# Kernel optimization log

Measured on AMD Instinct MI355X. Metric: run time of the kernel, lower is better.

The kernel has to match this reference:

```python
import jax, jax.numpy as jnp
import numpy as np

# ---- static config (mirrors DRR.__init__ kwargs) ----
NX = NY = NZ = 192            # volume dims
H = W = 192                   # detector height/width
SDR = 300.0                   # source-to-rotation-center distance
DELX = DELY = 2.0             # detector pixel pitch (mm)
X0 = Y0 = 0.0                 # detector offsets
SPACING = (1.0, 1.0, 1.0)     # voxel spacing (mm)
BAM = 1.0                     # bone_attenuation_multiplier
B = 2                         # batch (poses)
N_SUB = H * W // 2            # p_subsample = 0.5


def setup_inputs() -> dict:
    key = jax.random.key(0)
    k1, k2, k3, k4 = jax.random.split(key, 4)
    # CT volume in Hounsfield units, spanning air (-1000) to bone (~2000)
    volume = jax.random.uniform(k1, (NX, NY, NZ), jnp.float32, -1000.0, 2000.0)
    rotations = jax.random.normal(k2, (B, 3), jnp.float32)          # Euler ZYX (rad)
    translations = jax.random.normal(k3, (B, 3), jnp.float32) * 10.0  # mm, near isocenter
    # unique subsampled detector pixel indices (Detector.subsamples[-1])
    subsample_idx = jax.random.permutation(k4, H * W)[:N_SUB].astype(jnp.int32)
    return {"volume": volume, "rotations": rotations,
            "translations": translations, "subsample_idx": subsample_idx}


def _rz(t):
    c, s = jnp.cos(t), jnp.sin(t); z = jnp.zeros_like(t); o = jnp.ones_like(t)
    return jnp.stack([jnp.stack([c, -s, z], -1),
                      jnp.stack([s, c, z], -1),
                      jnp.stack([z, z, o], -1)], -2)


def _ry(t):
    c, s = jnp.cos(t), jnp.sin(t); z = jnp.zeros_like(t); o = jnp.ones_like(t)
    return jnp.stack([jnp.stack([c, z, s], -1),
                      jnp.stack([z, o, z], -1),
                      jnp.stack([-s, z, c], -1)], -2)


def _rx(t):
    c, s = jnp.cos(t), jnp.sin(t); z = jnp.zeros_like(t); o = jnp.ones_like(t)
    return jnp.stack([jnp.stack([o, z, z], -1),
                      jnp.stack([z, c, -s], -1),
                      jnp.stack([z, s, c], -1)], -2)


def _density(volume):
    # DRR.__init__: volume.flip([0]); air/soft/bone HU segmentation + normalization
    vol = jnp.flip(volume, 0)
    soft = (vol > -800.0) & (vol <= 350.0)
    soft_min = jnp.min(jnp.where(soft, vol, jnp.inf))
    d = jnp.where(vol <= -800.0, soft_min,
                  jnp.where(vol > 350.0, vol * BAM, vol))
    d = d - jnp.min(d)
    return d / jnp.max(d)


def _canonical_detector():
    # source on +z at SDR, detector plane at -z; pixel grid with pitch delx/dely
    xs = (jnp.arange(W, dtype=jnp.float32) - (W - 1) / 2.0) * DELX + X0
    ys = (jnp.arange(H, dtype=jnp.float32) - (H - 1) / 2.0) * DELY + Y0
    gy, gx = jnp.meshgrid(ys, xs, indexing="ij")
    tgt = jnp.stack([gx.ravel(), gy.ravel(),
                     jnp.full((H * W,), -SDR, jnp.float32)], -1)  # [H*W, 3]
    src = jnp.array([0.0, 0.0, SDR], jnp.float32)
    return src, tgt


def _siddon(density, source, target):
    """Siddon ray-casting. source [B,3], target [B,N,3] -> line integrals [B,N]."""
    dims = density.shape
    sp = jnp.asarray(SPACING, density.dtype)
    src = source[:, None, :]                     # [B,1,3]
    sdd = target - src                           # [B,N,3]
    sdd_safe = jnp.where(sdd == 0, 1e-9, sdd)
    # parametric intersections with all grid planes per axis
    alist = [(jnp.arange(dims[a] + 1, dtype=density.dtype)[None, None, :] * sp[a]
              - src[..., a:a + 1]) / sdd_safe[..., a:a + 1] for a in range(3)]
    a_first = jnp.stack([al[..., 0] for al in alist], -1)    # [B,N,3]
    a_last = jnp.stack([al[..., -1] for al in alist], -1)
    amin = jnp.maximum(jnp.max(jnp.minimum(a_first, a_last), -1), 0.0)[..., None]
    amax = jnp.minimum(jnp.min(jnp.maximum(a_first, a_last), -1), 1.0)[..., None]
    amax = jnp.maximum(amax, amin)               # ray misses -> zero-length segments
    alphas = jnp.sort(jnp.clip(jnp.concatenate(alist, -1), amin, amax), -1)  # [B,N,M+1]
    mid = 0.5 * (alphas[..., 1:] + alphas[..., :-1])                         # [B,N,M]
    ray_len = jnp.linalg.norm(target - src, axis=-1, keepdims=True)
    step = (alphas[..., 1:] - alphas[..., :-1]) * ray_len                    # [B,N,M]
    pts = src[..., None, :] + mid[..., None] * sdd[..., None, :]             # [B,N,M,3]
    idx = jnp.clip(jnp.floor(pts / sp).astype(jnp.int32), 0,
                   jnp.array(dims, jnp.int32) - 1)
    vox = density[idx[..., 0], idx[..., 1], idx[..., 2]]                     # gather
    return jnp.sum(step * vox, -1)


def reference(volume, rotations, translations, subsample_idx):
    density = _density(volume)
    src_c, tgt_c = _canonical_detector()
    tgt_c = tgt_c[subsample_idx]                                  # [N,3] subsampled rays
    R = _rz(rotations[:, 0]) @ _ry(rotations[:, 1]) @ _rx(rotations[:, 2])  # [B,3,3]
    center = jnp.array([NX, NY, NZ], jnp.float32) * jnp.asarray(SPACING, jnp.float32) / 2.0
    t = translations + center                                     # pose about isocenter
    source = jnp.einsum("bij,j->bi", R, src_c) + t                # [B,3]
    target = jnp.einsum("bij,nj->bni", R, tgt_c) + t[:, None, :]  # [B,N,3]
    img = _siddon(density, source, target)                        # [B,N]
    # reshape_subsampled_drr: scatter into zeros [B, H*W] then view [B,1,H,W]
    drr = jnp.zeros((img.shape[0], H * W), img.dtype).at[:, subsample_idx].set(img)
    return drr.reshape(-1, 1, H, W)
```

## Files before the change

kernel.cpp:

```cpp
#include <hip/hip_runtime.h>
#include <hip/hip_fp16.h>
#include <float.h>
#include <math.h>


#define NDIM   192
#define HW     (NDIM * NDIM)
#define NSUB   (HW / 2)
#define NTILE  576
#define NBATCH 2
#define NCHUNK 16
#define NVOX   (NDIM * NDIM * NDIM)
#define SDRF   300.0f
#define RBLK   1728

#define WS_LIST_OFF 16
#define WS_PART_OFF (16 + 4 * NSUB)
#define WS_DENS_OFF 98304

__global__ __launch_bounds__(256) void reduce_kernel(
    const float* __restrict__ vol, float* __restrict__ parts) {
    const int tid = blockIdx.x * 256 + threadIdx.x;
    const float4* __restrict__ v4 = (const float4*)vol;
    const int S = RBLK * 256;

    float4 r0 = v4[tid + 0 * S];
    float4 r1 = v4[tid + 1 * S];
    float4 r2 = v4[tid + 2 * S];
    float4 r3 = v4[tid + 3 * S];

    float smin = FLT_MAX, rmin = FLT_MAX, rmax = -FLT_MAX;
    float4 rr[4] = {r0, r1, r2, r3};
#pragma unroll
    for (int k = 0; k < 4; ++k) {
        float xs[4] = {rr[k].x, rr[k].y, rr[k].z, rr[k].w};
#pragma unroll
        for (int j = 0; j < 4; ++j) {
            float x = xs[j];
            bool in = (x > -800.0f);
            rmin = fminf(rmin, in ? x : FLT_MAX);
            rmax = fmaxf(rmax, in ? x : -FLT_MAX);
            smin = fminf(smin, (in && x <= 350.0f) ? x : FLT_MAX);
        }
    }
#pragma unroll
    for (int off = 32; off > 0; off >>= 1) {
        smin = fminf(smin, __shfl_down(smin, off));
        rmin = fminf(rmin, __shfl_down(rmin, off));
        rmax = fmaxf(rmax, __shfl_down(rmax, off));
    }
    __shared__ float sm[4], rm[4], rx[4];
    int w = threadIdx.x >> 6;
    if ((threadIdx.x & 63) == 0) { sm[w] = smin; rm[w] = rmin; rx[w] = rmax; }
    __syncthreads();
    if (threadIdx.x == 0) {
        parts[blockIdx.x] =
            fminf(fminf(sm[0], sm[1]), fminf(sm[2], sm[3]));
        parts[RBLK + blockIdx.x] =
            fminf(fminf(rm[0], rm[1]), fminf(rm[2], rm[3]));
        parts[2 * RBLK + blockIdx.x] =
            fmaxf(fmaxf(rx[0], rx[1]), fmaxf(rx[2], rx[3]));
    }
}

__device__ __forceinline__ int key_to_pixel(int tile, int lane) {
    int pi = (tile / 24) * 8 + (lane >> 3);
    int pj = (tile % 24) * 8 + (lane & 7);
    return pi * NDIM + pj;
}

__global__ __launch_bounds__(1024) void setup_kernel(
    const float* __restrict__ parts, const int* __restrict__ sidx,
    float* __restrict__ wsf, int* __restrict__ list) {
    __shared__ unsigned char smark[HW];
    __shared__ int s[NTILE];
    __shared__ float sm[16], rm[16], rx[16];
    const int t = threadIdx.x;

    int4* sm4 = (int4*)smark;
    for (int i = t; i < HW / 16; i += 1024) sm4[i] = make_int4(0, 0, 0, 0);

    float smin = FLT_MAX, rmin = FLT_MAX, rmax = -FLT_MAX;
    for (int i = t; i < RBLK; i += 1024) {
        smin = fminf(smin, parts[i]);
        rmin = fminf(rmin, parts[RBLK + i]);
        rmax = fmaxf(rmax, parts[2 * RBLK + i]);
    }
#pragma unroll
    for (int off = 32; off > 0; off >>= 1) {
        smin = fminf(smin, __shfl_down(smin, off));
        rmin = fminf(rmin, __shfl_down(rmin, off));
        rmax = fmaxf(rmax, __shfl_down(rmax, off));
    }
    int w = t >> 6;
    if ((t & 63) == 0) { sm[w] = smin; rm[w] = rmin; rx[w] = rmax; }
    __syncthreads();

    for (int i = t; i < NSUB; i += 1024) smark[sidx[i]] = 1;
    if (t == 0) {
        float a = FLT_MAX, b = FLT_MAX, c = -FLT_MAX;
#pragma unroll
        for (int k = 0; k < 16; ++k) {
            a = fminf(a, sm[k]); b = fminf(b, rm[k]); c = fmaxf(c, rx[k]);
        }
        wsf[0] = a; wsf[1] = b; wsf[2] = c;
    }
    __syncthreads();

    int cnt = 0;
    if (t < NTILE) {
#pragma unroll 8
        for (int lane = 0; lane < 64; ++lane)
            cnt += smark[key_to_pixel(t, lane)];
        s[t] = cnt;
    }
    __syncthreads();
    for (int off = 1; off < NTILE; off <<= 1) {
        int v = 0, u = 0;
        if (t < NTILE) {
            v = s[t];
            u = (t >= off) ? s[t - off] : 0;
        }
        __syncthreads();
        if (t < NTILE) s[t] = v + u;
        __syncthreads();
    }
    if (t < NTILE) {
        int pos = s[t] - cnt;
        for (int lane = 0; lane < 64; ++lane) {
            int p = key_to_pixel(t, lane);
            if (smark[p]) list[pos++] = p;
        }
    }
}

__global__ __launch_bounds__(256) void densify_kernel(
    const float* __restrict__ vol, const float* __restrict__ wsf,
    __half* __restrict__ dens) {
    const int t = blockIdx.x * 256 + threadIdx.x;
    const int o = t * 16;
    const int ox = o / HW;
    const int rem = o - ox * HW;

    float smin = wsf[0];
    float dmin = fminf(smin, wsf[1]);
    float scale = 1.0f / (fmaxf(smin, wsf[2]) - dmin);

    const float4* s4 = (const float4*)(vol + (NDIM - 1 - ox) * HW + rem);
    float4 a0 = s4[0], a1 = s4[1], a2 = s4[2], a3 = s4[3];
    float xs[16] = {a0.x, a0.y, a0.z, a0.w, a1.x, a1.y, a1.z, a1.w,
                    a2.x, a2.y, a2.z, a2.w, a3.x, a3.y, a3.z, a3.w};
    union { __half h[16]; int4 q[2]; } u;
#pragma unroll
    for (int k = 0; k < 16; ++k) {
        float v = xs[k];
        float d = (v <= -800.0f) ? smin : v;
        u.h[k] = __float2half_rn((d - dmin) * scale);
    }
    int4* d4 = (int4*)(dens + o);
    d4[0] = u.q[0];
    d4[1] = u.q[1];
}

__device__ __forceinline__ void init_axis(float s, float d, float a_lo,
                                          int& i, int& st, float& na) {
    if (d > 0.0f) {
        st = 1;
        float f = s + a_lo * d;
        int ii = (int)floorf(f) + 1;
        ii = max(0, min(ii, NDIM + 1));
        while (ii <= NDIM && ((float)ii - s) / d <= a_lo) ++ii;
        while (ii > 0 && ((float)(ii - 1) - s) / d > a_lo) --ii;
        i  = ii;
        na = (ii <= NDIM) ? ((float)ii - s) / d : FLT_MAX;
    } else {
        st = -1;
        float f = s + a_lo * d;
        int ii = (int)ceilf(f) - 1;
        ii = max(-1, min(ii, NDIM));
        while (ii >= 0 && ((float)ii - s) / d <= a_lo) --ii;
        while (ii < NDIM && ((float)(ii + 1) - s) / d > a_lo) ++ii;
        i  = ii;
        na = (ii >= 0) ? ((float)ii - s) / d : FLT_MAX;
    }
}

__global__ __launch_bounds__(256) void ray_kernel(
    const __half* __restrict__ dens, const float* __restrict__ rot,
    const float* __restrict__ trans, const int* __restrict__ list,
    float* __restrict__ out) {
    const int bid = blockIdx.x;
    const int xcd  = bid & 7;
    const int s_   = bid >> 3;
    const int b    = xcd >> 2;
    const int xr   = xcd & 3;
    const int c    = s_ & 15;
    const int pblk = s_ >> 4;
    const int n = (xr * 18 + pblk) * 256 + threadIdx.x;

    const int p  = list[n];
    const int pi = p / NDIM;
    const int pj = p % NDIM;

    float rz = rot[b * 3 + 0], ry = rot[b * 3 + 1], rx = rot[b * 3 + 2];
    float cz = cosf(rz), sz = sinf(rz);
    float cy = cosf(ry), sy = sinf(ry);
    float cx = cosf(rx), sx = sinf(rx);
    float R00 = cz * cy;
    float R01 = cz * sy * sx - sz * cx;
    float R02 = sz * sx + cz * sy * cx;
    float R10 = sz * cy;
    float R11 = cz * cx + sz * sy * sx;
    float R12 = sz * sy * cx - cz * sx;
    float R20 = -sy;
    float R21 = cy * sx;
    float R22 = cy * cx;
    float tx = trans[b * 3 + 0] + 96.0f;
    float ty = trans[b * 3 + 1] + 96.0f;
    float tz = trans[b * 3 + 2] + 96.0f;

    float srcx = R02 * SDRF + tx;
    float srcy = R12 * SDRF + ty;
    float srcz = R22 * SDRF + tz;
    float gx = ((float)pj - 95.5f) * 2.0f;
    float gy = ((float)pi - 95.5f) * 2.0f;
    float tgx = R00 * gx + R01 * gy + R02 * (-SDRF) + tx;
    float tgy = R10 * gx + R11 * gy + R12 * (-SDRF) + ty;
    float tgz = R20 * gx + R21 * gy + R22 * (-SDRF) + tz;

    float sdx = tgx - srcx, sdy = tgy - srcy, sdz = tgz - srcz;
    float dsx = (sdx == 0.0f) ? 1e-9f : sdx;
    float dsy = (sdy == 0.0f) ? 1e-9f : sdy;
    float dsz = (sdz == 0.0f) ? 1e-9f : sdz;

    float af0 = (0.0f - srcx) / dsx, al0 = (192.0f - srcx) / dsx;
    float af1 = (0.0f - srcy) / dsy, al1 = (192.0f - srcy) / dsy;
    float af2 = (0.0f - srcz) / dsz, al2 = (192.0f - srcz) / dsz;
    float amin = fmaxf(fmaxf(fminf(af0, al0), fminf(af1, al1)), fminf(af2, al2));
    amin = fmaxf(amin, 0.0f);
    float amax = fminf(fminf(fmaxf(af0, al0), fmaxf(af1, al1)), fmaxf(af2, al2));
    amax = fminf(amax, 1.0f);
    amax = fmaxf(amax, amin);
    float ray_len = sqrtf(sdx * sdx + sdy * sdy + sdz * sdz);

    float span = amax - amin;
    float a_lo = amin + span * ((float)c / (float)NCHUNK);
    float a_hi = (c == NCHUNK - 1) ? amax
                                   : amin + span * ((float)(c + 1) / (float)NCHUNK);

    int i0, i1, i2, st0, st1, st2;
    float na0, na1, na2;
    init_axis(srcx, dsx, a_lo, i0, st0, na0);
    init_axis(srcy, dsy, a_lo, i1, st1, na1);
    init_axis(srcz, dsz, a_lo, i2, st2, na2);

    float r0 = 1.0f / dsx, r1 = 1.0f / dsy, r2 = 1.0f / dsz;
    float fi0 = (float)i0, fi1 = (float)i1, fi2 = (float)i2;
    float fs0 = (float)st0, fs1 = (float)st1, fs2 = (float)st2;

    float cur = a_lo;
    float acc = 0.0f;

    auto compute_seg = [&](float& step, bool& fin, __half& hv) {
        float an = fminf(fminf(na0, na1), na2);
        fin = !(an < a_hi);
        float a2 = fin ? a_hi : an;
        float mid = 0.5f * (cur + a2);
        float px = fmaf(mid, sdx, srcx);
        float py = fmaf(mid, sdy, srcy);
        float pz = fmaf(mid, sdz, srcz);
        int ix = min(max((int)px, 0), NDIM - 1);
        int iy = min(max((int)py, 0), NDIM - 1);
        int iz = min(max((int)pz, 0), NDIM - 1);
        hv = dens[ix * HW + iy * NDIM + iz];
        bool c0 = (na0 == an), c1 = (na1 == an), c2 = (na2 == an);
        float nf0 = fi0 + fs0, nf1 = fi1 + fs1, nf2 = fi2 + fs2;
        float nn0 = (nf0 - srcx) * r0;
        float nn1 = (nf1 - srcy) * r1;
        float nn2 = (nf2 - srcz) * r2;
        fi0 = c0 ? nf0 : fi0;  na0 = c0 ? nn0 : na0;
        fi1 = c1 ? nf1 : fi1;  na1 = c1 ? nn1 : na1;
        fi2 = c2 ? nf2 : fi2;  na2 = c2 ? nn2 : na2;
        step = a2 - cur;
        cur = a2;
    };

    float stepA, stepB;
    bool  finA,  finB;
    __half hvA, hvB;
    compute_seg(stepA, finA, hvA);
    while (true) {
        if (finA) { acc = fmaf(stepA, __half2float(hvA), acc); break; }
        compute_seg(stepB, finB, hvB);
        acc = fmaf(stepA, __half2float(hvA), acc);
        if (finB) { acc = fmaf(stepB, __half2float(hvB), acc); break; }
        compute_seg(stepA, finA, hvA);
        acc = fmaf(stepB, __half2float(hvB), acc);
    }
    atomicAdd(&out[b * HW + p], acc * ray_len);
}

extern "C" void kernel_launch(void* const* d_in, const int* in_sizes, int n_in,
                              void* d_out, int out_size, void* d_ws,
                              size_t ws_size, hipStream_t stream) {
    const float* vol   = (const float*)d_in[0];
    const float* rot   = (const float*)d_in[1];
    const float* trans = (const float*)d_in[2];
    const int*   sidx  = (const int*)d_in[3];
    float* out = (float*)d_out;

    float*  wsf   = (float*)d_ws;
    int*    list  = (int*)((unsigned char*)d_ws + WS_LIST_OFF);
    float*  parts = (float*)((unsigned char*)d_ws + WS_PART_OFF);
    __half* dens  = (__half*)((unsigned char*)d_ws + WS_DENS_OFF);

    hipMemsetAsync(d_out, 0, (size_t)out_size * sizeof(float), stream);
    reduce_kernel<<<RBLK, 256, 0, stream>>>(vol, parts);
    setup_kernel<<<1, 1024, 0, stream>>>(parts, sidx, wsf, list);
    densify_kernel<<<RBLK, 256, 0, stream>>>(vol, wsf, dens);
    ray_kernel<<<NCHUNK * NBATCH * (NSUB / 256), 256, 0, stream>>>(
        dens, rot, trans, list, out);
}
```

Before: 139.5 us.

## Store half-precision density in 4x4x2 bricked layout for ray gather locality

```diff
diff --git a/kernel.cpp b/kernel.cpp
--- a/kernel.cpp
+++ b/kernel.cpp
@@ -13,6 +13,7 @@
 #define NVOX   (NDIM * NDIM * NDIM)
 #define SDRF   300.0f
 #define RBLK   1728
+#define NLINE  (NVOX / 32)
 
 #define WS_LIST_OFF 16
 #define WS_PART_OFF (16 + 4 * NSUB)
@@ -137,29 +138,32 @@
 __global__ __launch_bounds__(256) void densify_kernel(
     const float* __restrict__ vol, const float* __restrict__ wsf,
     __half* __restrict__ dens) {
-    const int t = blockIdx.x * 256 + threadIdx.x;
-    const int o = t * 16;
-    const int ox = o / HW;
-    const int rem = o - ox * HW;
+    const int g = blockIdx.x * 256 + threadIdx.x;
+    const int col = g / 96;
+    const int lin = g - col * 96;
+    const int IX = col / 48;
+    const int IY = col - IX * 48;
+    const int base_z = lin * 2;
 
     float smin = wsf[0];
     float dmin = fminf(smin, wsf[1]);
     float scale = 1.0f / (fmaxf(smin, wsf[2]) - dmin);
 
-    const float4* s4 = (const float4*)(vol + (NDIM - 1 - ox) * HW + rem);
-    float4 a0 = s4[0], a1 = s4[1], a2 = s4[2], a3 = s4[3];
-    float xs[16] = {a0.x, a0.y, a0.z, a0.w, a1.x, a1.y, a1.z, a1.w,
-                    a2.x, a2.y, a2.z, a2.w, a3.x, a3.y, a3.z, a3.w};
-    union { __half h[16]; int4 q[2]; } u;
-#pragma unroll
-    for (int k = 0; k < 16; ++k) {
-        float v = xs[k];
-        float d = (v <= -800.0f) ? smin : v;
-        u.h[k] = __float2half_rn((d - dmin) * scale);
-    }
-    int4* d4 = (int4*)(dens + o);
-    d4[0] = u.q[0];
-    d4[1] = u.q[1];
+    union { __half h[32]; int4 q[4]; } u;
+#pragma unroll
+    for (int r = 0; r < 16; ++r) {
+        int ixl = r >> 2, iyl = r & 3;
+        int ix = IX * 4 + ixl;
+        int iy = IY * 4 + iyl;
+        const float2 v2 = *(const float2*)(vol + (NDIM - 1 - ix) * HW
+                                               + iy * NDIM + base_z);
+        float d0 = (v2.x <= -800.0f) ? smin : v2.x;
+        float d1 = (v2.y <= -800.0f) ? smin : v2.y;
+        u.h[(r << 1) + 0] = __float2half_rn((d0 - dmin) * scale);
+        u.h[(r << 1) + 1] = __float2half_rn((d1 - dmin) * scale);
+    }
+    int4* d4 = (int4*)(dens + g * 32);
+    d4[0] = u.q[0]; d4[1] = u.q[1]; d4[2] = u.q[2]; d4[3] = u.q[3];
 }
 
 __device__ __forceinline__ void init_axis(float s, float d, float a_lo,
@@ -272,7 +276,9 @@
         int ix = min(max((int)px, 0), NDIM - 1);
         int iy = min(max((int)py, 0), NDIM - 1);
         int iz = min(max((int)pz, 0), NDIM - 1);
-        hv = dens[ix * HW + iy * NDIM + iz];
+        int addr = ((((ix >> 2) * 48 + (iy >> 2)) * 96 + (iz >> 1)) << 5)
+                 + ((ix & 3) << 3) + ((iy & 3) << 1) + (iz & 1);
+        hv = dens[addr];
         bool c0 = (na0 == an), c1 = (na1 == an), c2 = (na2 == an);
         float nf0 = fi0 + fs0, nf1 = fi1 + fs1, nf2 = fi2 + fs2;
         float nn0 = (nf0 - srcx) * r0;
@@ -317,7 +323,7 @@
     hipMemsetAsync(d_out, 0, (size_t)out_size * sizeof(float), stream);
     reduce_kernel<<<RBLK, 256, 0, stream>>>(vol, parts);
     setup_kernel<<<1, 1024, 0, stream>>>(parts, sidx, wsf, list);
-    densify_kernel<<<RBLK, 256, 0, stream>>>(vol, wsf, dens);
+    densify_kernel<<<NLINE / 256, 256, 0, stream>>>(vol, wsf, dens);
     ray_kernel<<<NCHUNK * NBATCH * (NSUB / 256), 256, 0, stream>>>(
         dens, rot, trans, list, out);
 }
```

New measurement: 131.0 us. -6.1%, faster.
